# Kernel optimization log

Measured on AMD Instinct MI355X. Metric: run time of the kernel, lower is better.

## Reference

```python
import jax, jax.numpy as jnp
import numpy as np

N_NODES = 50000
N_EDGES = 800000
D = 128          # in_feats == out_feats (residual connection)
E_DIMS = 128
NEG_SLOPE = 0.01  # F.leaky_relu default


def setup_inputs() -> dict:
    key = jax.random.key(0)
    ks = jax.random.split(key, 7)
    h = jax.random.normal(ks[0], (N_NODES, D), dtype=jnp.float32)
    edge_w = jax.random.normal(ks[1], (N_EDGES, E_DIMS), dtype=jnp.float32)
    W_self = jax.random.normal(ks[2], (D, D), dtype=jnp.float32) * (2.0 / D) ** 0.5
    W_func = jax.random.normal(ks[3], (D, D), dtype=jnp.float32) * (2.0 / D) ** 0.5
    W_att = jax.random.normal(ks[4], (1, 2 * D + E_DIMS), dtype=jnp.float32) * 0.1
    src = jax.random.randint(ks[5], (N_EDGES,), 0, N_NODES, dtype=jnp.int32)
    dst = jax.random.randint(ks[6], (N_EDGES,), 0, N_NODES, dtype=jnp.int32)
    return {"h": h, "edge_w": edge_w, "W_self": W_self, "W_func": W_func,
            "W_att": W_att, "src": src, "dst": dst}


def reference(h, edge_w, W_self, W_func, W_att, src, dst):
    N = h.shape[0]
    h_in = h
    h_s = h @ W_self.T                     # [N, D] self transform
    z = h @ W_func.T                       # [N, D] message transform

    # attention logit: leaky_relu(W_att @ [z_src, z_dst, e_w]) -- split the
    # single linear into per-node / per-edge pieces (same math, no big concat)
    wa = W_att[0]
    s_src = z @ wa[:D]                     # [N]
    s_dst = z @ wa[D:2 * D]                # [N]
    s_e = edge_w @ wa[2 * D:]              # [E]
    logits = jax.nn.leaky_relu(s_src[src] + s_dst[dst] + s_e, NEG_SLOPE)  # [E]

    # edge softmax grouped by destination node (ragged mailboxes)
    m = jax.ops.segment_max(logits, dst, num_segments=N)
    m = jnp.where(jnp.isfinite(m), m, 0.0)
    ex = jnp.exp(logits - m[dst])
    denom = jax.ops.segment_sum(ex, dst, num_segments=N)
    a = ex / jnp.maximum(denom[dst], 1e-9)                     # [E]

    # weighted scatter-sum of source messages
    agg = jax.ops.segment_sum(a[:, None] * z[src], dst, num_segments=N)  # [N, D]

    # DGL: nodes with zero in-degree keep their original ndata['h']
    deg = jax.ops.segment_sum(jnp.ones_like(logits), dst, num_segments=N)
    h_new = jnp.where(deg[:, None] > 0, h_s + agg, h_in)

    h_new = jax.nn.relu(h_new)             # relu=True
    return h_in + h_new                    # res_connection=True
```

## Files before the change

kernel.cpp:

```cpp
#include <hip/hip_runtime.h>
#include <hip/hip_bf16.h>
#include <math.h>

#define D 128
constexpr int NT = 64;

__global__ __launch_bounds__(256) void node_transform(
    const float* __restrict__ h, const float* __restrict__ Wf,
    const float* __restrict__ Ws, float* __restrict__ z,
    float* __restrict__ hs_out, int N)
{
    __shared__ float tile[NT * D];
    const int t = threadIdx.x;
    const int n0 = blockIdx.x * NT;
    const float* __restrict__ W = (blockIdx.y == 0) ? Wf : Ws;
    float* __restrict__ out = (blockIdx.y == 0) ? z : hs_out;
    const int nvalid = min(NT, N - n0);

    {
        const float4* __restrict__ src4 = (const float4*)(h + (size_t)n0 * D);
        float4* dst4 = (float4*)tile;
        #pragma unroll
        for (int i = 0; i < 8; ++i) {
            int idx = t + i * 256;
            float4 v = make_float4(0.f, 0.f, 0.f, 0.f);
            if ((idx >> 5) < nvalid) v = src4[idx];
            dst4[idx] = v;
        }
    }
    __syncthreads();

    const int oi = t & 31;
    const int q  = t >> 5;
    float acc[8][4];
    #pragma unroll
    for (int n = 0; n < 8; ++n)
        #pragma unroll
        for (int m = 0; m < 4; ++m) acc[n][m] = 0.f;

    for (int kk = 0; kk < D; kk += 8) {
        float4 w[4][2];
        #pragma unroll
        for (int m = 0; m < 4; ++m) {
            const float* wr = W + (size_t)(oi + 32 * m) * D + kk;
            w[m][0] = *(const float4*)wr;
            w[m][1] = *(const float4*)(wr + 4);
        }
        #pragma unroll
        for (int n = 0; n < 8; ++n) {
            const float* hp = &tile[(q * 8 + n) * D + kk];
            float4 a = *(const float4*)hp;
            float4 b = *(const float4*)(hp + 4);
            #pragma unroll
            for (int m = 0; m < 4; ++m) {
                acc[n][m] += a.x * w[m][0].x + a.y * w[m][0].y
                           + a.z * w[m][0].z + a.w * w[m][0].w
                           + b.x * w[m][1].x + b.y * w[m][1].y
                           + b.z * w[m][1].z + b.w * w[m][1].w;
            }
        }
    }

    #pragma unroll
    for (int n = 0; n < 8; ++n) {
        int node = q * 8 + n;
        if (node < nvalid) {
            float* op = out + (size_t)(n0 + node) * D + oi;
            #pragma unroll
            for (int m = 0; m < 4; ++m) op[32 * m] = acc[n][m];
        }
    }
}

__global__ __launch_bounds__(256) void node_scores(
    const float* __restrict__ z, const float* __restrict__ wa,
    float* __restrict__ s_src, float* __restrict__ s_dst, int N)
{
    const int lane = threadIdx.x & 63;
    const int n = blockIdx.x * 4 + (threadIdx.x >> 6);
    if (n >= N) return;
    float2 zv = *(const float2*)(z + (size_t)n * D + 2 * lane);
    float a = zv.x * wa[2 * lane]     + zv.y * wa[2 * lane + 1];
    float b = zv.x * wa[D + 2 * lane] + zv.y * wa[D + 2 * lane + 1];
    #pragma unroll
    for (int off = 32; off > 0; off >>= 1) {
        a += __shfl_xor(a, off, 64);
        b += __shfl_xor(b, off, 64);
    }
    if (lane == 0) { s_src[n] = a; s_dst[n] = b; }
}

__global__ __launch_bounds__(256) void edge_matvec_hist(
    const float* __restrict__ edge_w, const float* __restrict__ wa,
    const int* __restrict__ dst, float* __restrict__ s_e,
    int* __restrict__ deg, int E)
{
    const int lg = threadIdx.x & 15;
    const int g0 = (blockIdx.x * blockDim.x + threadIdx.x) >> 4;
    const int ng = (gridDim.x * blockDim.x) >> 4;
    const float4* wa4 = (const float4*)(wa + 2 * D);
    const float4 w0 = wa4[2 * lg];
    const float4 w1 = wa4[2 * lg + 1];
    for (int e = g0; e < E; e += ng) {
        const float4* ewp = (const float4*)(edge_w + (size_t)e * D);
        float4 a = ewp[2 * lg];
        float4 b = ewp[2 * lg + 1];
        float p = a.x * w0.x + a.y * w0.y + a.z * w0.z + a.w * w0.w
                + b.x * w1.x + b.y * w1.y + b.z * w1.z + b.w * w1.w;
        p += __shfl_xor(p, 1, 16);
        p += __shfl_xor(p, 2, 16);
        p += __shfl_xor(p, 4, 16);
        p += __shfl_xor(p, 8, 16);
        if (lg == 0) {
            s_e[e] = p;
            atomicAdd(deg + dst[e], 1);
        }
    }
}

__global__ __launch_bounds__(256) void scan_block_sums(
    const int* __restrict__ deg, int* __restrict__ bsum, int N)
{
    __shared__ int s[256];
    int i = blockIdx.x * 256 + threadIdx.x;
    s[threadIdx.x] = (i < N) ? deg[i] : 0;
    for (int o = 128; o > 0; o >>= 1) {
        __syncthreads();
        if (threadIdx.x < o) s[threadIdx.x] += s[threadIdx.x + o];
    }
    if (threadIdx.x == 0) bsum[blockIdx.x] = s[0];
}

__global__ __launch_bounds__(256) void scan_bsum(
    const int* __restrict__ bsum, int* __restrict__ boff, int NB)
{
    __shared__ int s[256];
    int t = threadIdx.x;
    int v = (t < NB) ? bsum[t] : 0;
    s[t] = v;
    for (int o = 1; o < 256; o <<= 1) {
        __syncthreads();
        int x = (t >= o) ? s[t - o] : 0;
        __syncthreads();
        s[t] += x;
    }
    __syncthreads();
    if (t < NB) boff[t] = s[t] - v;
}

__global__ __launch_bounds__(256) void scan_final(
    const int* __restrict__ deg, const int* __restrict__ boff,
    int* __restrict__ off, int* __restrict__ cursor, int N)
{
    __shared__ int s[256];
    int t = threadIdx.x;
    int i = blockIdx.x * 256 + t;
    int v = (i < N) ? deg[i] : 0;
    s[t] = v;
    for (int o = 1; o < 256; o <<= 1) {
        __syncthreads();
        int x = (t >= o) ? s[t - o] : 0;
        __syncthreads();
        s[t] += x;
    }
    __syncthreads();
    if (i < N) {
        int ex = boff[blockIdx.x] + s[t] - v;
        off[i] = ex;
        cursor[i] = ex;
    }
}

__global__ __launch_bounds__(256) void edge_scatter(
    const int* __restrict__ src, const int* __restrict__ dst,
    const float* __restrict__ s_src, const float* __restrict__ s_dst,
    const float* __restrict__ s_e, int* __restrict__ cursor,
    int2* __restrict__ bkt, int E)
{
    int e = blockIdx.x * blockDim.x + threadIdx.x;
    if (e >= E) return;
    int s = src[e];
    int d = dst[e];
    float logit = s_src[s] + s_dst[d] + s_e[e];
    logit = (logit > 0.f) ? logit : 0.01f * logit;
    float ex = __expf(logit);
    int pos = atomicAdd(cursor + d, 1);
    bkt[pos] = make_int2(s, __float_as_int(ex));
}

__global__ __launch_bounds__(256) void agg_finalize(
    const int* __restrict__ off, const int* __restrict__ deg,
    const int2* __restrict__ bkt, const float* __restrict__ z,
    const float* __restrict__ h, const float* __restrict__ h_s,
    float* __restrict__ out, int N)
{
    const int lane = threadIdx.x & 63;
    const int n = blockIdx.x * 4 + (threadIdx.x >> 6);
    if (n >= N) return;
    const int b  = off[n];
    const int dg = deg[n];
    float ax = 0.f, ay = 0.f, dsum = 0.f;
    int e = 0;
    for (; e + 8 <= dg; e += 8) {
        int2 p[8];
        #pragma unroll
        for (int j = 0; j < 8; ++j) p[j] = bkt[b + e + j];
        float2 zv[8];
        #pragma unroll
        for (int j = 0; j < 8; ++j)
            zv[j] = *(const float2*)(z + (size_t)p[j].x * D + 2 * lane);
        #pragma unroll
        for (int j = 0; j < 8; ++j) {
            float ex = __int_as_float(p[j].y);
            dsum += ex;
            ax += ex * zv[j].x;
            ay += ex * zv[j].y;
        }
    }
    for (; e < dg; ++e) {
        int2 p = bkt[b + e];
        float ex = __int_as_float(p.y);
        float2 zv = *(const float2*)(z + (size_t)p.x * D + 2 * lane);
        dsum += ex;
        ax += ex * zv.x;
        ay += ex * zv.y;
    }
    float2 hv = *(const float2*)(h + (size_t)n * D + 2 * lane);
    float rx, ry;
    if (dg > 0) {
        float inv = 1.f / fmaxf(dsum, 1e-9f);
        float2 hs = *(const float2*)(h_s + (size_t)n * D + 2 * lane);
        rx = hs.x + ax * inv;
        ry = hs.y + ay * inv;
    } else {
        rx = hv.x; ry = hv.y;
    }
    rx = fmaxf(rx, 0.f); ry = fmaxf(ry, 0.f);
    float2 o = make_float2(hv.x + rx, hv.y + ry);
    *(float2*)(out + (size_t)n * D + 2 * lane) = o;
}

extern "C" void kernel_launch(void* const* d_in, const int* in_sizes, int n_in,
                              void* d_out, int out_size, void* d_ws, size_t ws_size,
                              hipStream_t stream)
{
    const float* h      = (const float*)d_in[0];
    const float* edge_w = (const float*)d_in[1];
    const float* W_self = (const float*)d_in[2];
    const float* W_func = (const float*)d_in[3];
    const float* W_att  = (const float*)d_in[4];
    const int*   src    = (const int*)d_in[5];
    const int*   dst    = (const int*)d_in[6];
    float* out = (float*)d_out;

    const int N = in_sizes[0] / D;
    const int E = in_sizes[1] / D;
    const int NB = (N + 255) / 256;

    float* z     = (float*)d_ws;
    float* s_e   = z + (size_t)N * D;
    float* s_src = s_e + E;
    float* s_dst = s_src + N;
    int2*  bkt   = (int2*)(s_dst + N);
    int*   deg   = (int*)(bkt + E);
    int*   off   = deg + N;
    int*   cursor= off + N;
    int*   bsum  = cursor + N;
    int*   boff  = bsum + 256;

    hipMemsetAsync(deg, 0, (size_t)N * sizeof(int), stream);

    {
        dim3 grid((N + NT - 1) / NT, 2);
        node_transform<<<grid, 256, 0, stream>>>(h, W_func, W_self, z, out, N);
    }
    node_scores<<<(N + 3) / 4, 256, 0, stream>>>(z, W_att, s_src, s_dst, N);

    edge_matvec_hist<<<2048, 256, 0, stream>>>(edge_w, W_att, dst, s_e, deg, E);

    scan_block_sums<<<NB, 256, 0, stream>>>(deg, bsum, N);
    scan_bsum<<<1, 256, 0, stream>>>(bsum, boff, NB);
    scan_final<<<NB, 256, 0, stream>>>(deg, boff, off, cursor, N);

    edge_scatter<<<(E + 255) / 256, 256, 0, stream>>>(src, dst, s_src, s_dst,
                                                      s_e, cursor, bkt, E);

    agg_finalize<<<(N + 3) / 4, 256, 0, stream>>>(off, deg, bkt, z, h, out, out, N);
}
```

Before: 796.1 us.

## Fuse node scores into GEMM, merge edge score with scatter, store z as bf16

Computes s_src/s_dst inside the node transform epilogue through warp shuffles over a remapped output-row layout, which removes the separate node_scores kernel and its re-read of z. The degree histogram becomes a standalone vectorized kernel so the per-edge matvec can be fused with the bucket scatter, dropping the s_e round trip. z is stored packed as bf16 to halve gather traffic in aggregation, at the cost of lower precision in the messages.

```diff
diff --git a/kernel.cpp b/kernel.cpp
--- a/kernel.cpp
+++ b/kernel.cpp
@@ -1,20 +1,31 @@
 #include <hip/hip_runtime.h>
-#include <hip/hip_bf16.h>
 #include <math.h>
 
 #define D 128
 constexpr int NT = 64;
 
+static __device__ __forceinline__ unsigned bf16_rn(float x) {
+    unsigned u = __float_as_uint(x);
+    return (u + 0x7fffu + ((u >> 16) & 1u)) >> 16;
+}
+static __device__ __forceinline__ unsigned pack_bf16x2(float lo, float hi) {
+    return bf16_rn(lo) | (bf16_rn(hi) << 16);
+}
+static __device__ __forceinline__ float2 unpack_bf16x2(unsigned u) {
+    return make_float2(__uint_as_float(u << 16),
+                       __uint_as_float(u & 0xffff0000u));
+}
+
 __global__ __launch_bounds__(256) void node_transform(
     const float* __restrict__ h, const float* __restrict__ Wf,
-    const float* __restrict__ Ws, float* __restrict__ z,
-    float* __restrict__ hs_out, int N)
+    const float* __restrict__ Ws, const float* __restrict__ wa,
+    unsigned* __restrict__ zp, float* __restrict__ s_src,
+    float* __restrict__ s_dst, float* __restrict__ hs_out, int N)
 {
     __shared__ float tile[NT * D];
     const int t = threadIdx.x;
     const int n0 = blockIdx.x * NT;
     const float* __restrict__ W = (blockIdx.y == 0) ? Wf : Ws;
-    float* __restrict__ out = (blockIdx.y == 0) ? z : hs_out;
     const int nvalid = min(NT, N - n0);
 
     {
@@ -32,6 +43,8 @@
 
     const int oi = t & 31;
     const int q  = t >> 5;
+    const int rows[4] = { 2 * oi, 2 * oi + 1, 64 + 2 * oi, 64 + 2 * oi + 1 };
+
     float acc[8][4];
     #pragma unroll
     for (int n = 0; n < 8; ++n)
@@ -42,7 +55,7 @@
         float4 w[4][2];
         #pragma unroll
         for (int m = 0; m < 4; ++m) {
-            const float* wr = W + (size_t)(oi + 32 * m) * D + kk;
+            const float* wr = W + (size_t)rows[m] * D + kk;
             w[m][0] = *(const float4*)wr;
             w[m][1] = *(const float4*)(wr + 4);
         }
@@ -61,39 +74,126 @@
         }
     }
 
-    #pragma unroll
-    for (int n = 0; n < 8; ++n) {
-        int node = q * 8 + n;
-        if (node < nvalid) {
-            float* op = out + (size_t)(n0 + node) * D + oi;
+    if (blockIdx.y == 0) {
+        #pragma unroll
+        for (int n = 0; n < 8; ++n) {
+            int node = q * 8 + n;
+            if (node < nvalid) {
+                unsigned* op = zp + (size_t)(n0 + node) * 64;
+                op[oi]      = pack_bf16x2(acc[n][0], acc[n][1]);
+                op[32 + oi] = pack_bf16x2(acc[n][2], acc[n][3]);
+            }
+        }
+        const float ws0 = wa[rows[0]],     ws1 = wa[rows[1]];
+        const float ws2 = wa[rows[2]],     ws3 = wa[rows[3]];
+        const float wd0 = wa[D + rows[0]], wd1 = wa[D + rows[1]];
+        const float wd2 = wa[D + rows[2]], wd3 = wa[D + rows[3]];
+        #pragma unroll
+        for (int n = 0; n < 8; ++n) {
+            float ps = acc[n][0] * ws0 + acc[n][1] * ws1
+                     + acc[n][2] * ws2 + acc[n][3] * ws3;
+            float pd = acc[n][0] * wd0 + acc[n][1] * wd1
+                     + acc[n][2] * wd2 + acc[n][3] * wd3;
             #pragma unroll
-            for (int m = 0; m < 4; ++m) op[32 * m] = acc[n][m];
-        }
-    }
-}
-
-__global__ __launch_bounds__(256) void node_scores(
-    const float* __restrict__ z, const float* __restrict__ wa,
-    float* __restrict__ s_src, float* __restrict__ s_dst, int N)
-{
-    const int lane = threadIdx.x & 63;
-    const int n = blockIdx.x * 4 + (threadIdx.x >> 6);
-    if (n >= N) return;
-    float2 zv = *(const float2*)(z + (size_t)n * D + 2 * lane);
-    float a = zv.x * wa[2 * lane]     + zv.y * wa[2 * lane + 1];
-    float b = zv.x * wa[D + 2 * lane] + zv.y * wa[D + 2 * lane + 1];
-    #pragma unroll
-    for (int off = 32; off > 0; off >>= 1) {
-        a += __shfl_xor(a, off, 64);
-        b += __shfl_xor(b, off, 64);
-    }
-    if (lane == 0) { s_src[n] = a; s_dst[n] = b; }
-}
-
-__global__ __launch_bounds__(256) void edge_matvec_hist(
+            for (int off = 16; off > 0; off >>= 1) {
+                ps += __shfl_xor(ps, off, 32);
+                pd += __shfl_xor(pd, off, 32);
+            }
+            int node = q * 8 + n;
+            if (oi == 0 && node < nvalid) {
+                s_src[n0 + node] = ps;
+                s_dst[n0 + node] = pd;
+            }
+        }
+    } else {
+        #pragma unroll
+        for (int n = 0; n < 8; ++n) {
+            int node = q * 8 + n;
+            if (node < nvalid) {
+                float* op = hs_out + (size_t)(n0 + node) * D;
+                *(float2*)(op + 2 * oi)      = make_float2(acc[n][0], acc[n][1]);
+                *(float2*)(op + 64 + 2 * oi) = make_float2(acc[n][2], acc[n][3]);
+            }
+        }
+    }
+}
+
+__global__ __launch_bounds__(256) void deg_hist(
+    const int* __restrict__ dst, int* __restrict__ deg, int E)
+{
+    int tid = blockIdx.x * blockDim.x + threadIdx.x;
+    int stride = gridDim.x * blockDim.x;
+    int E4 = E >> 2;
+    const int4* d4 = (const int4*)dst;
+    for (int i = tid; i < E4; i += stride) {
+        int4 v = d4[i];
+        atomicAdd(deg + v.x, 1);
+        atomicAdd(deg + v.y, 1);
+        atomicAdd(deg + v.z, 1);
+        atomicAdd(deg + v.w, 1);
+    }
+    for (int e = (E4 << 2) + tid; e < E; e += stride)
+        atomicAdd(deg + dst[e], 1);
+}
+
+__global__ __launch_bounds__(256) void scan_block_sums(
+    const int* __restrict__ deg, int* __restrict__ bsum, int N)
+{
+    __shared__ int s[256];
+    int i = blockIdx.x * 256 + threadIdx.x;
+    s[threadIdx.x] = (i < N) ? deg[i] : 0;
+    for (int o = 128; o > 0; o >>= 1) {
+        __syncthreads();
+        if (threadIdx.x < o) s[threadIdx.x] += s[threadIdx.x + o];
+    }
+    if (threadIdx.x == 0) bsum[blockIdx.x] = s[0];
+}
+
+__global__ __launch_bounds__(256) void scan_bsum(
+    const int* __restrict__ bsum, int* __restrict__ boff, int NB)
+{
+    __shared__ int s[256];
+    int t = threadIdx.x;
+    int v = (t < NB) ? bsum[t] : 0;
+    s[t] = v;
+    for (int o = 1; o < 256; o <<= 1) {
+        __syncthreads();
+        int x = (t >= o) ? s[t - o] : 0;
+        __syncthreads();
+        s[t] += x;
+    }
+    __syncthreads();
+    if (t < NB) boff[t] = s[t] - v;
+}
+
+__global__ __launch_bounds__(256) void scan_final(
+    const int* __restrict__ deg, const int* __restrict__ boff,
+    int* __restrict__ off, int* __restrict__ cursor, int N)
+{
+    __shared__ int s[256];
+    int t = threadIdx.x;
+    int i = blockIdx.x * 256 + t;
+    int v = (i < N) ? deg[i] : 0;
+    s[t] = v;
+    for (int o = 1; o < 256; o <<= 1) {
+        __syncthreads();
+        int x = (t >= o) ? s[t - o] : 0;
+        __syncthreads();
+        s[t] += x;
+    }
+    __syncthreads();
+    if (i < N) {
+        int ex = boff[blockIdx.x] + s[t] - v;
+        off[i] = ex;
+        cursor[i] = ex;
+    }
+}
+
+__global__ __launch_bounds__(256) void edge_score_scatter(
     const float* __restrict__ edge_w, const float* __restrict__ wa,
-    const int* __restrict__ dst, float* __restrict__ s_e,
-    int* __restrict__ deg, int E)
+    const int* __restrict__ src, const int* __restrict__ dst,
+    const float* __restrict__ s_src, const float* __restrict__ s_dst,
+    int* __restrict__ cursor, int2* __restrict__ bkt, int E)
 {
     const int lg = threadIdx.x & 15;
     const int g0 = (blockIdx.x * blockDim.x + threadIdx.x) >> 4;
@@ -112,85 +212,20 @@
         p += __shfl_xor(p, 4, 16);
         p += __shfl_xor(p, 8, 16);
         if (lg == 0) {
-            s_e[e] = p;
-            atomicAdd(deg + dst[e], 1);
-        }
-    }
-}
-
-__global__ __launch_bounds__(256) void scan_block_sums(
-    const int* __restrict__ deg, int* __restrict__ bsum, int N)
-{
-    __shared__ int s[256];
-    int i = blockIdx.x * 256 + threadIdx.x;
-    s[threadIdx.x] = (i < N) ? deg[i] : 0;
-    for (int o = 128; o > 0; o >>= 1) {
-        __syncthreads();
-        if (threadIdx.x < o) s[threadIdx.x] += s[threadIdx.x + o];
-    }
-    if (threadIdx.x == 0) bsum[blockIdx.x] = s[0];
-}
-
-__global__ __launch_bounds__(256) void scan_bsum(
-    const int* __restrict__ bsum, int* __restrict__ boff, int NB)
-{
-    __shared__ int s[256];
-    int t = threadIdx.x;
-    int v = (t < NB) ? bsum[t] : 0;
-    s[t] = v;
-    for (int o = 1; o < 256; o <<= 1) {
-        __syncthreads();
-        int x = (t >= o) ? s[t - o] : 0;
-        __syncthreads();
-        s[t] += x;
-    }
-    __syncthreads();
-    if (t < NB) boff[t] = s[t] - v;
-}
-
-__global__ __launch_bounds__(256) void scan_final(
-    const int* __restrict__ deg, const int* __restrict__ boff,
-    int* __restrict__ off, int* __restrict__ cursor, int N)
-{
-    __shared__ int s[256];
-    int t = threadIdx.x;
-    int i = blockIdx.x * 256 + t;
-    int v = (i < N) ? deg[i] : 0;
-    s[t] = v;
-    for (int o = 1; o < 256; o <<= 1) {
-        __syncthreads();
-        int x = (t >= o) ? s[t - o] : 0;
-        __syncthreads();
-        s[t] += x;
-    }
-    __syncthreads();
-    if (i < N) {
-        int ex = boff[blockIdx.x] + s[t] - v;
-        off[i] = ex;
-        cursor[i] = ex;
-    }
-}
-
-__global__ __launch_bounds__(256) void edge_scatter(
-    const int* __restrict__ src, const int* __restrict__ dst,
-    const float* __restrict__ s_src, const float* __restrict__ s_dst,
-    const float* __restrict__ s_e, int* __restrict__ cursor,
-    int2* __restrict__ bkt, int E)
-{
-    int e = blockIdx.x * blockDim.x + threadIdx.x;
-    if (e >= E) return;
-    int s = src[e];
-    int d = dst[e];
-    float logit = s_src[s] + s_dst[d] + s_e[e];
-    logit = (logit > 0.f) ? logit : 0.01f * logit;
-    float ex = __expf(logit);
-    int pos = atomicAdd(cursor + d, 1);
-    bkt[pos] = make_int2(s, __float_as_int(ex));
+            int s = src[e];
+            int d = dst[e];
+            float logit = s_src[s] + s_dst[d] + p;
+            logit = (logit > 0.f) ? logit : 0.01f * logit;
+            float ex = __expf(logit);
+            int pos = atomicAdd(cursor + d, 1);
+            bkt[pos] = make_int2(s, __float_as_int(ex));
+        }
+    }
 }
 
 __global__ __launch_bounds__(256) void agg_finalize(
     const int* __restrict__ off, const int* __restrict__ deg,
-    const int2* __restrict__ bkt, const float* __restrict__ z,
+    const int2* __restrict__ bkt, const unsigned* __restrict__ zp,
     const float* __restrict__ h, const float* __restrict__ h_s,
     float* __restrict__ out, int N)
 {
@@ -205,25 +240,26 @@
         int2 p[8];
         #pragma unroll
         for (int j = 0; j < 8; ++j) p[j] = bkt[b + e + j];
-        float2 zv[8];
+        unsigned zv[8];
         #pragma unroll
         for (int j = 0; j < 8; ++j)
-            zv[j] = *(const float2*)(z + (size_t)p[j].x * D + 2 * lane);
+            zv[j] = zp[(size_t)p[j].x * 64 + lane];
         #pragma unroll
         for (int j = 0; j < 8; ++j) {
             float ex = __int_as_float(p[j].y);
+            float2 z2 = unpack_bf16x2(zv[j]);
             dsum += ex;
-            ax += ex * zv[j].x;
-            ay += ex * zv[j].y;
+            ax += ex * z2.x;
+            ay += ex * z2.y;
         }
     }
     for (; e < dg; ++e) {
         int2 p = bkt[b + e];
         float ex = __int_as_float(p.y);
-        float2 zv = *(const float2*)(z + (size_t)p.x * D + 2 * lane);
+        float2 z2 = unpack_bf16x2(zp[(size_t)p.x * 64 + lane]);
         dsum += ex;
-        ax += ex * zv.x;
-        ay += ex * zv.y;
+        ax += ex * z2.x;
+        ay += ex * z2.y;
     }
     float2 hv = *(const float2*)(h + (size_t)n * D + 2 * lane);
     float rx, ry;
@@ -257,33 +293,31 @@
     const int E = in_sizes[1] / D;
     const int NB = (N + 255) / 256;
 
-    float* z     = (float*)d_ws;
-    float* s_e   = z + (size_t)N * D;
-    float* s_src = s_e + E;
-    float* s_dst = s_src + N;
-    int2*  bkt   = (int2*)(s_dst + N);
-    int*   deg   = (int*)(bkt + E);
-    int*   off   = deg + N;
-    int*   cursor= off + N;
-    int*   bsum  = cursor + N;
-    int*   boff  = bsum + 256;
+    unsigned* zp  = (unsigned*)d_ws;
+    float* s_src  = (float*)(zp + (size_t)N * 64);
+    float* s_dst  = s_src + N;
+    int2*  bkt    = (int2*)(s_dst + N);
+    int*   deg    = (int*)(bkt + E);
+    int*   off    = deg + N;
+    int*   cursor = off + N;
+    int*   bsum   = cursor + N;
+    int*   boff   = bsum + 256;
 
     hipMemsetAsync(deg, 0, (size_t)N * sizeof(int), stream);
 
-    {
-        dim3 grid((N + NT - 1) / NT, 2);
-        node_transform<<<grid, 256, 0, stream>>>(h, W_func, W_self, z, out, N);
-    }
-    node_scores<<<(N + 3) / 4, 256, 0, stream>>>(z, W_att, s_src, s_dst, N);
-
-    edge_matvec_hist<<<2048, 256, 0, stream>>>(edge_w, W_att, dst, s_e, deg, E);
-
+    deg_hist<<<1024, 256, 0, stream>>>(dst, deg, E);
     scan_block_sums<<<NB, 256, 0, stream>>>(deg, bsum, N);
     scan_bsum<<<1, 256, 0, stream>>>(bsum, boff, NB);
     scan_final<<<NB, 256, 0, stream>>>(deg, boff, off, cursor, N);
 
-    edge_scatter<<<(E + 255) / 256, 256, 0, stream>>>(src, dst, s_src, s_dst,
-                                                      s_e, cursor, bkt, E);
-
-    agg_finalize<<<(N + 3) / 4, 256, 0, stream>>>(off, deg, bkt, z, h, out, out, N);
-}
+    {
+        dim3 grid((N + NT - 1) / NT, 2);
+        node_transform<<<grid, 256, 0, stream>>>(h, W_func, W_self, W_att,
+                                                 zp, s_src, s_dst, out, N);
+    }
+
+    edge_score_scatter<<<2048, 256, 0, stream>>>(edge_w, W_att, src, dst,
+                                                 s_src, s_dst, cursor, bkt, E);
+
+    agg_finalize<<<(N + 3) / 4, 256, 0, stream>>>(off, deg, bkt, zp, h, out, out, N);
+}
```

After: 781.5 us. Within noise of the previous version (-1.8%).
